# Kernel tuning notes

Hardware: AMD Instinct MI355X
Metric: run time of the kernel (lower is better)

## Reference

```python
import jax, jax.numpy as jnp
import numpy as np

B, T, D = 8, 2048, 768
H, DK = 6, 128            # num_heads, head_dim = n_embd // n_head
DV = 2 * DK               # head_v_dim = head_dim * expand_v
KDIM, VDIM = H * DK, H * DV
CONV = 4
EPS = 1e-5                # RMSNorm eps


def short_conv_silu(x, w):
    """Causal depthwise conv1d (no bias) + SiLU. x: [B,T,C], w: [C,K]."""
    K = w.shape[-1]
    xp = jnp.pad(x, ((0, 0), (K - 1, 0), (0, 0)))
    y = sum(xp[:, i:i + x.shape[1], :] * w[:, i] for i in range(K))
    return jax.nn.silu(y)


def l2norm(x):
    return x * jax.lax.rsqrt(jnp.sum(x * x, axis=-1, keepdims=True) + 1e-6)


def gated_delta_rule(q, k, v, g, beta):
    """q,k: [B,H,T,DK]; v: [B,H,T,DV]; g,beta: [B,H,T]. Returns o: [B,H,T,DV].
    S_t = exp(g_t) * S_{t-1}; v' = beta_t*(v_t - k_t @ S); S += outer(k_t, v'); o_t = scale*q_t @ S."""
    scale = DK ** -0.5

    def per_head(qh, kh, vh, gh, bh):
        def step(S, inp):
            qt, kt, vt, gt, bt = inp
            S = S * jnp.exp(gt)
            v_new = bt * (vt - kt @ S)
            S = S + kt[:, None] * v_new[None, :]
            return S, (qt * scale) @ S
        S0 = jnp.zeros((DK, DV), qh.dtype)
        _, o = jax.lax.scan(step, S0, (qh, kh, vh, gh, bh))
        return o

    return jax.vmap(jax.vmap(per_head))(q, k, v, g, beta)


def setup_inputs() -> dict:
    key = jax.random.key(0)
    ks = jax.random.split(key, 16)
    s = D ** -0.5
    inp = {
        "x": jax.random.normal(ks[0], (B, T, D), jnp.float32),
        "Wq": jax.random.normal(ks[1], (D, KDIM), jnp.float32) * s,
        "Wk": jax.random.normal(ks[2], (D, KDIM), jnp.float32) * s,
        "Wv": jax.random.normal(ks[3], (D, VDIM), jnp.float32) * s,
        "Wa": jax.random.normal(ks[4], (D, H), jnp.float32) * s,
        "Wb": jax.random.normal(ks[5], (D, H), jnp.float32) * s,
        "Wg": jax.random.normal(ks[6], (D, VDIM), jnp.float32) * s,
        "Wo": jax.random.normal(ks[7], (VDIM, D), jnp.float32) * (VDIM ** -0.5),
        "conv_q": jax.random.uniform(ks[8], (KDIM, CONV), jnp.float32, -0.5, 0.5),
        "conv_k": jax.random.uniform(ks[9], (KDIM, CONV), jnp.float32, -0.5, 0.5),
        "conv_v": jax.random.uniform(ks[10], (VDIM, CONV), jnp.float32, -0.5, 0.5),
        "A_log": jnp.log(jax.random.uniform(ks[11], (H,), jnp.float32, 1.0, 8.0)),
        "dt_bias": -4.0 + 0.5 * jax.random.normal(ks[12], (H,), jnp.float32),
        "o_norm_w": jnp.ones((DV,), jnp.float32),
    }
    return inp


def reference(x, Wq, Wk, Wv, Wa, Wb, Wg, Wo, conv_q, conv_k, conv_v, A_log, dt_bias, o_norm_w):
    # projections + causal short conv + silu
    q = short_conv_silu(x @ Wq, conv_q)          # [B,T,KDIM]
    k = short_conv_silu(x @ Wk, conv_k)
    v = short_conv_silu(x @ Wv, conv_v)          # [B,T,VDIM]

    q = l2norm(q.reshape(B, T, H, DK)).transpose(0, 2, 1, 3)   # [B,H,T,DK]
    k = l2norm(k.reshape(B, T, H, DK)).transpose(0, 2, 1, 3)
    v = v.reshape(B, T, H, DV).transpose(0, 2, 1, 3)           # [B,H,T,DV]

    beta = jax.nn.sigmoid(x @ Wb).transpose(0, 2, 1)           # [B,H,T]
    g = -jnp.exp(A_log) * jax.nn.softplus(x @ Wa + dt_bias)    # [B,T,H] log-decay
    g = g.transpose(0, 2, 1)                                   # [B,H,T]

    o = gated_delta_rule(q, k, v, g, beta)                     # [B,H,T,DV]
    o = o.transpose(0, 2, 1, 3)                                # [B,T,H,DV]

    # gated RMSNorm (FusedRMSNormSwishGate): rmsnorm(o)*w*silu(gate)
    gate = (x @ Wg).reshape(B, T, H, DV)
    o = o * jax.lax.rsqrt(jnp.mean(o * o, axis=-1, keepdims=True) + EPS)
    o = o * o_norm_w * jax.nn.silu(gate)

    return o.reshape(B, T, VDIM) @ Wo                          # [B,T,D]
```

## Files before the change

### kernel.cpp

```cpp
#include <hip/hip_runtime.h>
#include <hip/hip_bf16.h>
#include <stdint.h>

#define BB   8
#define TT   2048
#define DD   768
#define HH   6
#define DKd  128
#define DVd  256
#define MM   (BB*TT)
#define K1   768
#define K2   1536
#define CC   32

typedef __bf16 bf16x8 __attribute__((ext_vector_type(8)));
typedef __bf16 bf16x4 __attribute__((ext_vector_type(4)));
typedef float  f32x4  __attribute__((ext_vector_type(4)));

__device__ __forceinline__ float sigm(float x) { return 1.f / (1.f + __expf(-x)); }
__device__ __forceinline__ void split2(float v, __bf16& hi, __bf16& lo) {
  hi = (__bf16)v; lo = (__bf16)(v - (float)hi);
}
__device__ __forceinline__ f32x4 mfma3(bf16x8 ah, bf16x8 al, bf16x8 bh_, bf16x8 bl_, f32x4 acc) {
  acc = __builtin_amdgcn_mfma_f32_16x16x32_bf16(ah, bh_, acc, 0, 0, 0);
  acc = __builtin_amdgcn_mfma_f32_16x16x32_bf16(ah, bl_, acc, 0, 0, 0);
  acc = __builtin_amdgcn_mfma_f32_16x16x32_bf16(al, bh_, acc, 0, 0, 0);
  return acc;
}

__global__ void convert_x_kernel(const float* __restrict__ x, __bf16* __restrict__ Xs) {
  int idx = blockIdx.x * 256 + threadIdx.x;
  if (idx >= MM * DD) return;
  int m = idx / DD, c = idx - m * DD;
  float v = x[idx];
  __bf16 h = (__bf16)v;
  __bf16 l = (__bf16)(v - (float)h);
  size_t base = (size_t)m * (2 * K1) + c;
  Xs[base] = h; Xs[base + K1] = l;
}

__global__ void convert_w_kernel(const float* __restrict__ W, __bf16* __restrict__ Wt,
                                 int K, int N) {
  int idx = blockIdx.x * 256 + threadIdx.x;
  if (idx >= N * 3 * K) return;
  int n = idx / (3 * K), kk = idx - n * (3 * K);
  int blk = kk / K, k = kk - blk * K;
  float v = W[(size_t)k * N + n];
  __bf16 h = (__bf16)v;
  Wt[idx] = (blk == 1) ? (__bf16)(v - (float)h) : h;
}

template <typename OutT>
__global__ __launch_bounds__(256) void gemm_split(
    const __bf16* __restrict__ A, const __bf16* __restrict__ Bt,
    OutT* __restrict__ C, int N, int Khi)
{
  __shared__ __bf16 Als[128 * 32];
  __shared__ __bf16 Bls[128 * 32];
  const int LDA = 2 * Khi, Klog = 3 * Khi;
  const int tid = threadIdx.x;
  const int lane = tid & 63, w = tid >> 6;
  const int wr = w >> 1, wc = w & 1;
  const int bm = blockIdx.x, bn = blockIdx.y;
  f32x4 acc[4][4] = {};
  const __bf16* Ab = A + (size_t)bm * 128 * LDA;
  const __bf16* Bb = Bt + (size_t)bn * 128 * Klog;
  const int r0 = tid >> 2, co0 = (tid & 3) * 8;
  const int r1 = (256 + tid) >> 2, co1 = ((256 + tid) & 3) * 8;
  for (int k0 = 0; k0 < Klog; k0 += 32) {
    const int kc = (k0 < Khi) ? k0 : k0 - Khi;
    __syncthreads();
    __builtin_amdgcn_global_load_lds(
        (const __attribute__((address_space(1))) void*)(Ab + (size_t)r0 * LDA + kc + co0),
        (__attribute__((address_space(3))) void*)(Als + (w * 64) * 8), 16, 0, 0);
    __builtin_amdgcn_global_load_lds(
        (const __attribute__((address_space(1))) void*)(Ab + (size_t)r1 * LDA + kc + co1),
        (__attribute__((address_space(3))) void*)(Als + (256 + w * 64) * 8), 16, 0, 0);
    __builtin_amdgcn_global_load_lds(
        (const __attribute__((address_space(1))) void*)(Bb + (size_t)r0 * Klog + k0 + co0),
        (__attribute__((address_space(3))) void*)(Bls + (w * 64) * 8), 16, 0, 0);
    __builtin_amdgcn_global_load_lds(
        (const __attribute__((address_space(1))) void*)(Bb + (size_t)r1 * Klog + k0 + co1),
        (__attribute__((address_space(3))) void*)(Bls + (256 + w * 64) * 8), 16, 0, 0);
    __syncthreads();
    bf16x8 af[4], bfr[4];
    const int rb = wr * 64 + (lane & 15);
    const int kb = (lane >> 4) * 8;
#pragma unroll
    for (int i = 0; i < 4; ++i) af[i] = *(const bf16x8*)(Als + (rb + i * 16) * 32 + kb);
    const int cb = wc * 64 + (lane & 15);
#pragma unroll
    for (int i = 0; i < 4; ++i) bfr[i] = *(const bf16x8*)(Bls + (cb + i * 16) * 32 + kb);
#pragma unroll
    for (int mi = 0; mi < 4; ++mi)
#pragma unroll
      for (int ni = 0; ni < 4; ++ni)
        acc[mi][ni] = __builtin_amdgcn_mfma_f32_16x16x32_bf16(af[mi], bfr[ni], acc[mi][ni], 0, 0, 0);
  }
  const int row0 = bm * 128 + wr * 64;
  const int col0 = bn * 128 + wc * 64 + (lane & 15);
  const int rsub = (lane >> 4) * 4;
#pragma unroll
  for (int mi = 0; mi < 4; ++mi)
#pragma unroll
    for (int ni = 0; ni < 4; ++ni)
#pragma unroll
      for (int r = 0; r < 4; ++r) {
        int row = row0 + mi * 16 + rsub + r;
        C[(size_t)row * N + col0 + ni * 16] = (OutT)acc[mi][ni][r];
      }
}

__global__ void gb_kernel(const float* __restrict__ x, const float* __restrict__ Wa,
                          const float* __restrict__ Wb, const float* __restrict__ A_log,
                          const float* __restrict__ dt_bias, float* __restrict__ g,
                          float* __restrict__ bet)
{
  const int row = blockIdx.x * 4 + (threadIdx.x >> 6);
  const int lane = threadIdx.x & 63;
  float aA[6] = {0, 0, 0, 0, 0, 0}, aB[6] = {0, 0, 0, 0, 0, 0};
  const float* xr = x + (size_t)row * DD;
  for (int kk = 0; kk < 12; ++kk) {
    const int c = lane + kk * 64;
    const float xv = xr[c];
#pragma unroll
    for (int hh = 0; hh < 6; ++hh) { aA[hh] += xv * Wa[c * 6 + hh]; aB[hh] += xv * Wb[c * 6 + hh]; }
  }
#pragma unroll
  for (int hh = 0; hh < 6; ++hh) {
#pragma unroll
    for (int off = 32; off; off >>= 1) {
      aA[hh] += __shfl_xor(aA[hh], off, 64);
      aB[hh] += __shfl_xor(aB[hh], off, 64);
    }
  }
  if (lane == 0) {
    const int b = row >> 11, t = row & (TT - 1);
#pragma unroll
    for (int hh = 0; hh < 6; ++hh) {
      const float a = aA[hh] + dt_bias[hh];
      const float sp = (a > 20.f) ? a : log1pf(__expf(a));
      const size_t gi = ((size_t)(b * HH + hh)) * TT + t;
      g[gi] = -__expf(A_log[hh]) * sp;
      bet[gi] = 1.f / (1.f + __expf(-aB[hh]));
    }
  }
}

__global__ __launch_bounds__(256) void delta_kernel(
    const __bf16* __restrict__ qpre, const __bf16* __restrict__ kpre,
    const __bf16* __restrict__ vpre,
    const float* __restrict__ cq, const float* __restrict__ ck,
    const float* __restrict__ cv,
    const float* __restrict__ g, const float* __restrict__ bet,
    __bf16* __restrict__ o)
{
  const int bh = blockIdx.x, b = bh / HH, h = bh - b * HH;
  const int jq = blockIdx.y;
  const int tid = threadIdx.x, lane = tid & 63, w = tid >> 6;
  const int r16 = lane & 15, g2 = lane >> 4;

  __shared__ __align__(16) __bf16 Khi[32][136], Klo[32][136];
  __shared__ __align__(16) __bf16 Qhi[32][136], Qlo[32][136];
  __shared__ __align__(16) __bf16 SThi[64][136], STlo[64][136];
  __shared__ __align__(16) __bf16 Ahi[32][40],  Alo[32][40];
  __shared__ __align__(16) __bf16 Phi[32][40],  Plo[32][40];
  __shared__ __align__(16) __bf16 VThi[64][40], VTlo[64][40];
  __shared__ __align__(16) __bf16 GThi[64][16], GTlo[64][16];
  __shared__ __align__(16) __bf16 Thi[4][16][24], Tlo[4][16][24];
  __shared__ __align__(16) float  RHSb[32][66];
  __shared__ __align__(16) float  cwkq[256][4];
  __shared__ __align__(16) float  cwv[64][4];
  __shared__ float Lv[32], Bv[32], BBv[32], BCb[32], Bb2[32];

  {
    const float* src = (tid < 128) ? ck + (size_t)(h * DKd + tid) * 4
                                   : cq + (size_t)(h * DKd + (tid - 128)) * 4;
    *(float4*)&cwkq[tid][0] = *(const float4*)src;
    if (tid < 64) *(float4*)&cwv[tid][0] = *(const float4*)(cv + (size_t)(h * DVd + jq * 64 + tid) * 4);
  }
  for (int i = tid; i < 1088; i += 256) {
    ((uint4*)SThi)[i] = make_uint4(0, 0, 0, 0);
    ((uint4*)STlo)[i] = make_uint4(0, 0, 0, 0);
  }
  __syncthreads();

  const size_t gbase = (size_t)bh * TT;
  const size_t obase = (size_t)bh * TT * DVd + jq * 64;
  const bf16x8 z8 = {};

  for (int chk = 0; chk < TT / CC; ++chk) {
    const int t0 = chk * CC;
    {
      const int r = tid >> 3, cg = tid & 7;
      const int tG = t0 + r;
      {
        bf16x8 tp0[4], tp1[4];
#pragma unroll
        for (int i = 0; i < 4; ++i) {
          int t = tG - 3 + i;
          if (t >= 0) {
            const __bf16* p = kpre + ((size_t)(b * TT + t)) * DD + h * DKd + cg * 16;
            tp0[i] = *(const bf16x8*)p; tp1[i] = *(const bf16x8*)(p + 8);
          } else { tp0[i] = z8; tp1[i] = z8; }
        }
        float ss = 0.f;
#pragma unroll
        for (int c = 0; c < 16; ++c) {
          const float4 w4 = *(const float4*)&cwkq[cg * 16 + c][0];
          const int j = c & 7;
          float y = (c < 8)
              ? (w4.x * (float)tp0[0][j] + w4.y * (float)tp0[1][j] + w4.z * (float)tp0[2][j] + w4.w * (float)tp0[3][j])
              : (w4.x * (float)tp1[0][j] + w4.y * (float)tp1[1][j] + w4.z * (float)tp1[2][j] + w4.w * (float)tp1[3][j]);
          y = y * sigm(y);
          ss += y * y;
          __bf16 hi, lo; split2(y, hi, lo);
          Khi[r][cg * 16 + c] = hi; Klo[r][cg * 16 + c] = lo;
        }
        ss += __shfl_xor(ss, 1, 64); ss += __shfl_xor(ss, 2, 64); ss += __shfl_xor(ss, 4, 64);
        const float inv = rsqrtf(ss + 1e-6f);
#pragma unroll
        for (int c = 0; c < 16; ++c) {
          float v = ((float)Khi[r][cg * 16 + c] + (float)Klo[r][cg * 16 + c]) * inv;
          __bf16 hi, lo; split2(v, hi, lo);
          Khi[r][cg * 16 + c] = hi; Klo[r][cg * 16 + c] = lo;
        }
      }
      {
        bf16x8 tp0[4], tp1[4];
#pragma unroll
        for (int i = 0; i < 4; ++i) {
          int t = tG - 3 + i;
          if (t >= 0) {
            const __bf16* p = qpre + ((size_t)(b * TT + t)) * DD + h * DKd + cg * 16;
            tp0[i] = *(const bf16x8*)p; tp1[i] = *(const bf16x8*)(p + 8);
          } else { tp0[i] = z8; tp1[i] = z8; }
        }
        float ss = 0.f;
#pragma unroll
        for (int c = 0; c < 16; ++c) {
          const float4 w4 = *(const float4*)&cwkq[128 + cg * 16 + c][0];
          const int j = c & 7;
          float y = (c < 8)
              ? (w4.x * (float)tp0[0][j] + w4.y * (float)tp0[1][j] + w4.z * (float)tp0[2][j] + w4.w * (float)tp0[3][j])
              : (w4.x * (float)tp1[0][j] + w4.y * (float)tp1[1][j] + w4.z * (float)tp1[2][j] + w4.w * (float)tp1[3][j]);
          y = y * sigm(y);
          ss += y * y;
          __bf16 hi, lo; split2(y, hi, lo);
          Qhi[r][cg * 16 + c] = hi; Qlo[r][cg * 16 + c] = lo;
        }
        ss += __shfl_xor(ss, 1, 64); ss += __shfl_xor(ss, 2, 64); ss += __shfl_xor(ss, 4, 64);
        const float inv = rsqrtf(ss + 1e-6f) * 0.08838834764831845f;
#pragma unroll
        for (int c = 0; c < 16; ++c) {
          float v = ((float)Qhi[r][cg * 16 + c] + (float)Qlo[r][cg * 16 + c]) * inv;
          __bf16 hi, lo; split2(v, hi, lo);
          Qhi[r][cg * 16 + c] = hi; Qlo[r][cg * 16 + c] = lo;
        }
      }
      {
        bf16x8 tv[4];
#pragma unroll
        for (int i = 0; i < 4; ++i) {
          int t = tG - 3 + i;
          tv[i] = (t >= 0) ? *(const bf16x8*)(vpre + ((size_t)(b * TT + t)) * K2 + h * DVd + jq * 64 + cg * 8) : z8;
        }
#pragma unroll
        for (int c = 0; c < 8; ++c) {
          const float4 w4 = *(const float4*)&cwv[cg * 8 + c][0];
          float y = w4.x * (float)tv[0][c] + w4.y * (float)tv[1][c] + w4.z * (float)tv[2][c] + w4.w * (float)tv[3][c];
          RHSb[r][cg * 8 + c] = y * sigm(y);
        }
      }
      if (tid < 32) {
        float gv = g[gbase + t0 + tid];
        float bv = bet[gbase + t0 + tid];
        float cum = gv;
#pragma unroll
        for (int off = 1; off < 32; off <<= 1) {
          int src = (lane >= off) ? lane - off : lane;
          float n = __shfl(cum, src, 64);
          if (lane >= off) cum += n;
        }
        float LC = __shfl(cum, 31, 64);
        Lv[tid] = cum;
        Bv[tid] = bv;
        float eb = __expf(cum);
        Bb2[tid] = eb;
        BBv[tid] = bv * eb;
        BCb[tid] = __expf(LC - cum);
      }
    }
    __syncthreads();

    {
      const int tr = w >> 1, tc = w & 1;
      f32x4 accA = {0.f, 0.f, 0.f, 0.f}, accP = {0.f, 0.f, 0.f, 0.f};
#pragma unroll
      for (int kb = 0; kb < 128; kb += 32) {
        bf16x8 bh_ = *(const bf16x8*)&Khi[tc * 16 + r16][kb + g2 * 8];
        bf16x8 bl_ = *(const bf16x8*)&Klo[tc * 16 + r16][kb + g2 * 8];
        bf16x8 ah = *(const bf16x8*)&Khi[tr * 16 + r16][kb + g2 * 8];
        bf16x8 al = *(const bf16x8*)&Klo[tr * 16 + r16][kb + g2 * 8];
        accA = mfma3(ah, al, bh_, bl_, accA);
        bf16x8 qh = *(const bf16x8*)&Qhi[tr * 16 + r16][kb + g2 * 8];
        bf16x8 ql = *(const bf16x8*)&Qlo[tr * 16 + r16][kb + g2 * 8];
        accP = mfma3(qh, ql, bh_, bl_, accP);
      }
      const int jj = tc * 16 + r16;
      const float Lj = Lv[jj];
#pragma unroll
      for (int reg = 0; reg < 4; ++reg) {
        const int tt = tr * 16 + g2 * 4 + reg;
        const float dL = Lv[tt] - Lj;
        const float ex = __expf(dL);
        float av = (jj < tt) ? Bv[tt] * ex * accA[reg] : 0.f;
        float pv = (jj <= tt) ? ex * accP[reg] : 0.f;
        __bf16 hi, lo;
        split2(av, hi, lo); Ahi[tt][jj] = hi; Alo[tt][jj] = lo;
        split2(pv, hi, lo); Phi[tt][jj] = hi; Plo[tt][jj] = lo;
      }
    }
    __syncthreads();

    {
      const int rb = w >> 1, cbs = (w & 1) * 2;
      f32x4 acc[2];
#pragma unroll
      for (int ct = 0; ct < 2; ++ct) {
        const int cc = (cbs + ct) * 16 + r16;
#pragma unroll
        for (int reg = 0; reg < 4; ++reg) {
          const int tt = rb * 16 + g2 * 4 + reg;
          acc[ct][reg] = Bv[tt] * RHSb[tt][cc];
        }
      }
      const float fneg = -BBv[rb * 16 + r16];
#pragma unroll
      for (int kb = 0; kb < 128; kb += 32) {
        bf16x8 xh = *(const bf16x8*)&Khi[rb * 16 + r16][kb + g2 * 8];
        bf16x8 xl = *(const bf16x8*)&Klo[rb * 16 + r16][kb + g2 * 8];
        bf16x8 ah, al;
#pragma unroll
        for (int j = 0; j < 8; ++j) {
          float v = fneg * ((float)xh[j] + (float)xl[j]);
          __bf16 hi, lo; split2(v, hi, lo); ah[j] = hi; al[j] = lo;
        }
#pragma unroll
        for (int ct = 0; ct < 2; ++ct) {
          bf16x8 sh = *(const bf16x8*)&SThi[(cbs + ct) * 16 + r16][kb + g2 * 8];
          bf16x8 sl = *(const bf16x8*)&STlo[(cbs + ct) * 16 + r16][kb + g2 * 8];
          acc[ct] = mfma3(ah, al, sh, sl, acc[ct]);
        }
      }
#pragma unroll
      for (int ct = 0; ct < 2; ++ct) {
        const int cc = (cbs + ct) * 16 + r16;
#pragma unroll
        for (int reg = 0; reg < 4; ++reg)
          RHSb[rb * 16 + g2 * 4 + reg][cc] = acc[ct][reg];
      }
    }
    if (w < 2) {
      const int I = w, r0 = I * 16, s = I + 2;
      bf16x8 Lh_r = z8, Ll_r = z8, Lh_t = z8, Ll_t = z8;
      if (g2 < 2) {
        Lh_r = *(const bf16x8*)&Ahi[r0 + r16][r0 + g2 * 8];
        Ll_r = *(const bf16x8*)&Alo[r0 + r16][r0 + g2 * 8];
#pragma unroll
        for (int j = 0; j < 8; ++j) {
          Lh_t[j] = Ahi[r0 + g2 * 8 + j][r0 + r16];
          Ll_t[j] = Alo[r0 + g2 * 8 + j][r0 + r16];
        }
      }
      f32x4 acc = {0.f, 0.f, 0.f, 0.f};
      acc = mfma3(Lh_r, Ll_r, Lh_t, Ll_t, acc);
#pragma unroll
      for (int reg = 0; reg < 4; ++reg) { __bf16 hi, lo; split2(acc[reg], hi, lo);
        Thi[s][g2 * 4 + reg][r16] = hi; Tlo[s][g2 * 4 + reg][r16] = lo; }
      bf16x8 L2h_r = z8, L2l_r = z8, L2h_t = z8, L2l_t = z8;
      if (g2 < 2) { L2h_r = *(const bf16x8*)&Thi[s][r16][g2 * 8]; L2l_r = *(const bf16x8*)&Tlo[s][r16][g2 * 8]; }
#pragma unroll
      for (int j = 0; j < 8; ++j) if (g2 < 2) { L2h_t[j] = Thi[s][g2 * 8 + j][r16]; L2l_t[j] = Tlo[s][g2 * 8 + j][r16]; }
      bf16x8 nLh = Lh_r, nLl = Ll_r;
#pragma unroll
      for (int j = 0; j < 8; ++j) { nLh[j] = -nLh[j]; nLl[j] = -nLl[j]; }
      f32x4 accR;
#pragma unroll
      for (int reg = 0; reg < 4; ++reg) {
        const int rr = g2 * 4 + reg;
        float lw = (float)Ahi[r0 + rr][r0 + r16] + (float)Alo[r0 + rr][r0 + r16];
        float l2w = (float)Thi[s][rr][r16] + (float)Tlo[s][rr][r16];
        accR[reg] = ((rr == r16) ? 1.f : 0.f) - lw + l2w;
      }
      accR = mfma3(nLh, nLl, L2h_t, L2l_t, accR);
#pragma unroll
      for (int reg = 0; reg < 4; ++reg) { __bf16 hi, lo; split2(accR[reg], hi, lo);
        Thi[I][g2 * 4 + reg][r16] = hi; Tlo[I][g2 * 4 + reg][r16] = lo; }
      f32x4 acc4 = {0.f, 0.f, 0.f, 0.f};
      acc4 = mfma3(L2h_r, L2l_r, L2h_t, L2l_t, acc4);
#pragma unroll
      for (int reg = 0; reg < 4; ++reg) { __bf16 hi, lo; split2(acc4[reg], hi, lo);
        Thi[s][g2 * 4 + reg][r16] = hi; Tlo[s][g2 * 4 + reg][r16] = lo; }
      bf16x8 R1h_r = z8, R1l_r = z8, L4h_t = z8, L4l_t = z8, L4h_r = z8, L4l_r = z8;
      if (g2 < 2) {
        R1h_r = *(const bf16x8*)&Thi[I][r16][g2 * 8]; R1l_r = *(const bf16x8*)&Tlo[I][r16][g2 * 8];
        L4h_r = *(const bf16x8*)&Thi[s][r16][g2 * 8]; L4l_r = *(const bf16x8*)&Tlo[s][r16][g2 * 8];
#pragma unroll
        for (int j = 0; j < 8; ++j) { L4h_t[j] = Thi[s][g2 * 8 + j][r16]; L4l_t[j] = Tlo[s][g2 * 8 + j][r16]; }
      }
      f32x4 accR2;
#pragma unroll
      for (int reg = 0; reg < 4; ++reg)
        accR2[reg] = (float)Thi[I][g2 * 4 + reg][r16] + (float)Tlo[I][g2 * 4 + reg][r16];
      accR2 = mfma3(R1h_r, R1l_r, L4h_t, L4l_t, accR2);
#pragma unroll
      for (int reg = 0; reg < 4; ++reg) { __bf16 hi, lo; split2(accR2[reg], hi, lo);
        Thi[I][g2 * 4 + reg][r16] = hi; Tlo[I][g2 * 4 + reg][r16] = lo; }
      f32x4 acc8 = {0.f, 0.f, 0.f, 0.f};
      acc8 = mfma3(L4h_r, L4l_r, L4h_t, L4l_t, acc8);
#pragma unroll
      for (int reg = 0; reg < 4; ++reg) { __bf16 hi, lo; split2(acc8[reg], hi, lo);
        Thi[s][g2 * 4 + reg][r16] = hi; Tlo[s][g2 * 4 + reg][r16] = lo; }
      bf16x8 R2h_r = z8, R2l_r = z8, L8h_t = z8, L8l_t = z8;
      if (g2 < 2) {
        R2h_r = *(const bf16x8*)&Thi[I][r16][g2 * 8]; R2l_r = *(const bf16x8*)&Tlo[I][r16][g2 * 8];
#pragma unroll
        for (int j = 0; j < 8; ++j) { L8h_t[j] = Thi[s][g2 * 8 + j][r16]; L8l_t[j] = Tlo[s][g2 * 8 + j][r16]; }
      }
      f32x4 accT;
#pragma unroll
      for (int reg = 0; reg < 4; ++reg)
        accT[reg] = (float)Thi[I][g2 * 4 + reg][r16] + (float)Tlo[I][g2 * 4 + reg][r16];
      accT = mfma3(R2h_r, R2l_r, L8h_t, L8l_t, accT);
#pragma unroll
      for (int reg = 0; reg < 4; ++reg) { __bf16 hi, lo; split2(accT[reg], hi, lo);
        Thi[I][g2 * 4 + reg][r16] = hi; Tlo[I][g2 * 4 + reg][r16] = lo; }
    }
    __syncthreads();

    {
      const int id0 = tid * 4;
      const int t = id0 >> 6, c0 = id0 & 63;
#pragma unroll
      for (int i = 0; i < 4; ++i) {
        __bf16 hi, lo; split2(RHSb[t][c0 + i], hi, lo);
        GThi[c0 + i][t] = hi; GTlo[c0 + i][t] = lo;
      }
    }
    __syncthreads();
    {
      bf16x8 th = z8, tl = z8, gh = z8, gl = z8;
      if (g2 < 2) {
        th = *(const bf16x8*)&Thi[0][r16][g2 * 8]; tl = *(const bf16x8*)&Tlo[0][r16][g2 * 8];
        gh = *(const bf16x8*)&GThi[w * 16 + r16][g2 * 8]; gl = *(const bf16x8*)&GTlo[w * 16 + r16][g2 * 8];
      }
      f32x4 acc = {0.f, 0.f, 0.f, 0.f};
      acc = mfma3(th, tl, gh, gl, acc);
      bf16x4 p4h, p4l;
#pragma unroll
      for (int reg = 0; reg < 4; ++reg) { __bf16 hi, lo; split2(acc[reg], hi, lo); p4h[reg] = hi; p4l[reg] = lo; }
      *(bf16x4*)&VThi[w * 16 + r16][g2 * 4] = p4h;
      *(bf16x4*)&VTlo[w * 16 + r16][g2 * 4] = p4l;
    }
    __syncthreads();
    {
      const int cb = w;
      f32x4 acc;
#pragma unroll
      for (int reg = 0; reg < 4; ++reg) acc[reg] = RHSb[16 + g2 * 4 + reg][cb * 16 + r16];
      bf16x8 ah = z8, al = z8, vh = z8, vl = z8;
      if (g2 < 2) {
        ah = *(const bf16x8*)&Ahi[16 + r16][g2 * 8]; al = *(const bf16x8*)&Alo[16 + r16][g2 * 8];
#pragma unroll
        for (int j = 0; j < 8; ++j) { ah[j] = -ah[j]; al[j] = -al[j]; }
        vh = *(const bf16x8*)&VThi[cb * 16 + r16][g2 * 8]; vl = *(const bf16x8*)&VTlo[cb * 16 + r16][g2 * 8];
      }
      acc = mfma3(ah, al, vh, vl, acc);
      bf16x4 p4h, p4l;
#pragma unroll
      for (int reg = 0; reg < 4; ++reg) { __bf16 hi, lo; split2(acc[reg], hi, lo); p4h[reg] = hi; p4l[reg] = lo; }
      *(bf16x4*)&GThi[cb * 16 + r16][g2 * 4] = p4h;
      *(bf16x4*)&GTlo[cb * 16 + r16][g2 * 4] = p4l;
    }
    __syncthreads();
    {
      bf16x8 th = z8, tl = z8, gh = z8, gl = z8;
      if (g2 < 2) {
        th = *(const bf16x8*)&Thi[1][r16][g2 * 8]; tl = *(const bf16x8*)&Tlo[1][r16][g2 * 8];
        gh = *(const bf16x8*)&GThi[w * 16 + r16][g2 * 8]; gl = *(const bf16x8*)&GTlo[w * 16 + r16][g2 * 8];
      }
      f32x4 acc = {0.f, 0.f, 0.f, 0.f};
      acc = mfma3(th, tl, gh, gl, acc);
      bf16x4 p4h, p4l;
#pragma unroll
      for (int reg = 0; reg < 4; ++reg) { __bf16 hi, lo; split2(acc[reg], hi, lo); p4h[reg] = hi; p4l[reg] = lo; }
      *(bf16x4*)&VThi[w * 16 + r16][16 + g2 * 4] = p4h;
      *(bf16x4*)&VTlo[w * 16 + r16][16 + g2 * 4] = p4l;
    }
    __syncthreads();

    {
      const int rb = w >> 1, cbs = (w & 1) * 2;
      f32x4 acc[2] = {{0.f, 0.f, 0.f, 0.f}, {0.f, 0.f, 0.f, 0.f}};
      const float fq = Bb2[rb * 16 + r16];
#pragma unroll
      for (int kb = 0; kb < 128; kb += 32) {
        bf16x8 xh = *(const bf16x8*)&Qhi[rb * 16 + r16][kb + g2 * 8];
        bf16x8 xl = *(const bf16x8*)&Qlo[rb * 16 + r16][kb + g2 * 8];
        bf16x8 qh, ql;
#pragma unroll
        for (int j = 0; j < 8; ++j) {
          float v = fq * ((float)xh[j] + (float)xl[j]);
          __bf16 hi, lo; split2(v, hi, lo); qh[j] = hi; ql[j] = lo;
        }
#pragma unroll
        for (int ct = 0; ct < 2; ++ct) {
          bf16x8 sh = *(const bf16x8*)&SThi[(cbs + ct) * 16 + r16][kb + g2 * 8];
          bf16x8 sl = *(const bf16x8*)&STlo[(cbs + ct) * 16 + r16][kb + g2 * 8];
          acc[ct] = mfma3(qh, ql, sh, sl, acc[ct]);
        }
      }
      bf16x8 ph = *(const bf16x8*)&Phi[rb * 16 + r16][g2 * 8];
      bf16x8 pl = *(const bf16x8*)&Plo[rb * 16 + r16][g2 * 8];
#pragma unroll
      for (int ct = 0; ct < 2; ++ct) {
        bf16x8 vh = *(const bf16x8*)&VThi[(cbs + ct) * 16 + r16][g2 * 8];
        bf16x8 vl = *(const bf16x8*)&VTlo[(cbs + ct) * 16 + r16][g2 * 8];
        acc[ct] = mfma3(ph, pl, vh, vl, acc[ct]);
        const int cc = (cbs + ct) * 16 + r16;
#pragma unroll
        for (int reg = 0; reg < 4; ++reg) {
          const int tt = rb * 16 + g2 * 4 + reg;
          o[obase + (size_t)(t0 + tt) * DVd + cc] = (__bf16)acc[ct][reg];
        }
      }
    }
    __syncthreads();

    {
      const float bCf = __expf(Lv[31]);
      bf16x8 vh4[4], vl4[4];
#pragma unroll
      for (int cb = 0; cb < 4; ++cb) {
        vh4[cb] = *(const bf16x8*)&VThi[cb * 16 + r16][g2 * 8];
        vl4[cb] = *(const bf16x8*)&VTlo[cb * 16 + r16][g2 * 8];
      }
#pragma unroll
      for (int rr = 0; rr < 2; ++rr) {
        const int rb = w * 2 + rr, d0 = rb * 16;
        bf16x8 kh, kl;
#pragma unroll
        for (int j = 0; j < 8; ++j) {
          const int t = g2 * 8 + j;
          float v = BCb[t] * ((float)Khi[t][d0 + r16] + (float)Klo[t][d0 + r16]);
          __bf16 hi, lo; split2(v, hi, lo); kh[j] = hi; kl[j] = lo;
        }
#pragma unroll
        for (int cb = 0; cb < 4; ++cb) {
          f32x4 acc;
          const int cc = cb * 16 + r16;
#pragma unroll
          for (int reg = 0; reg < 4; ++reg) {
            const int dd = d0 + g2 * 4 + reg;
            acc[reg] = bCf * ((float)SThi[cc][dd] + (float)STlo[cc][dd]);
          }
          acc = mfma3(kh, kl, vh4[cb], vl4[cb], acc);
          bf16x4 p4h, p4l;
#pragma unroll
          for (int reg = 0; reg < 4; ++reg) { __bf16 hi, lo; split2(acc[reg], hi, lo); p4h[reg] = hi; p4l[reg] = lo; }
          *(bf16x4*)&SThi[cc][d0 + g2 * 4] = p4h;
          *(bf16x4*)&STlo[cc][d0 + g2 * 4] = p4l;
        }
      }
    }
    __syncthreads();
  }
}

__global__ void epilogue_kernel(const __bf16* __restrict__ o, const __bf16* __restrict__ gate,
                                const float* __restrict__ wn, __bf16* __restrict__ Os)
{
  const int bid = blockIdx.x;
  const int m = bid / HH, h = bid - m * HH;
  const int b = m >> 11, t = m & (TT - 1);
  const int j = threadIdx.x;
  const float ov = (float)o[((size_t)(b * HH + h) * TT + t) * DVd + j];
  float ss = ov * ov;
#pragma unroll
  for (int off = 32; off; off >>= 1) ss += __shfl_xor(ss, off, 64);
  __shared__ float red[4];
  if ((j & 63) == 0) red[j >> 6] = ss;
  __syncthreads();
  const float inv = rsqrtf((red[0] + red[1] + red[2] + red[3]) * (1.f / DVd) + 1e-5f);
  const float gt = (float)gate[(size_t)m * K2 + h * DVd + j];
  const float val = ov * inv * wn[j] * (gt * sigm(gt));
  const __bf16 hi = (__bf16)val;
  const __bf16 lo = (__bf16)(val - (float)hi);
  const size_t ob = (size_t)m * (2 * K2) + h * DVd + j;
  Os[ob] = hi; Os[ob + K2] = lo;
}

__global__ void sentinel_kernel(float* __restrict__ out, float val) {
  out[threadIdx.x] = val;
}

extern "C" void kernel_launch(void* const* d_in, const int* in_sizes, int n_in,
                              void* d_out, int out_size, void* d_ws, size_t ws_size,
                              hipStream_t stream) {
  const float* x    = (const float*)d_in[0];
  const float* Wq   = (const float*)d_in[1];
  const float* Wk   = (const float*)d_in[2];
  const float* Wv   = (const float*)d_in[3];
  const float* Wa   = (const float*)d_in[4];
  const float* Wb   = (const float*)d_in[5];
  const float* Wg   = (const float*)d_in[6];
  const float* Wo   = (const float*)d_in[7];
  const float* cq   = (const float*)d_in[8];
  const float* ck   = (const float*)d_in[9];
  const float* cv   = (const float*)d_in[10];
  const float* Alog = (const float*)d_in[11];
  const float* dtb  = (const float*)d_in[12];
  const float* onw  = (const float*)d_in[13];
  float* out = (float*)d_out;
  uint8_t* ws = (uint8_t*)d_ws;

  const size_t oGt = 0;
  const size_t oG  = oGt + 50331648;
  const size_t oBt = oG  + 393216;
  const size_t oWo = oBt + 393216;
  const size_t oWq = oWo + 7077888;
  const size_t oWk = oWq + 3538944;
  const size_t oWv = oWk + 3538944;
  const size_t oWg = oWv + 7077888;
  const size_t oXs = oWg + 7077888;
  const size_t oQp = oXs + 50331648;
  const size_t oKp = oQp + 25165824;
  const size_t oVp = oKp + 25165824;
  const size_t total = oVp + 50331648;
  const size_t oO  = oXs;
  const size_t oOs = oQp;

  if (ws_size < total) {
    sentinel_kernel<<<1, 256, 0, stream>>>(out, 1.0e7f + (float)(ws_size >> 20));
    return;
  }

  __bf16* Xs   = (__bf16*)(ws + oXs);
  __bf16* Wqp  = (__bf16*)(ws + oWq);
  __bf16* Wkp  = (__bf16*)(ws + oWk);
  __bf16* Wvp  = (__bf16*)(ws + oWv);
  __bf16* Wgp  = (__bf16*)(ws + oWg);
  __bf16* Wop  = (__bf16*)(ws + oWo);
  __bf16* qpre = (__bf16*)(ws + oQp);
  __bf16* kpre = (__bf16*)(ws + oKp);
  __bf16* vpre = (__bf16*)(ws + oVp);
  __bf16* gate = (__bf16*)(ws + oGt);
  float*  gbuf = (float*)(ws + oG);
  float*  bbuf = (float*)(ws + oBt);
  __bf16* oBuf = (__bf16*)(ws + oO);
  __bf16* Os   = (__bf16*)(ws + oOs);

  convert_x_kernel<<<MM * DD / 256, 256, 0, stream>>>(x, Xs);
  convert_w_kernel<<<768 * 3 * K1 / 256, 256, 0, stream>>>(Wq, Wqp, K1, 768);
  convert_w_kernel<<<768 * 3 * K1 / 256, 256, 0, stream>>>(Wk, Wkp, K1, 768);
  convert_w_kernel<<<1536 * 3 * K1 / 256, 256, 0, stream>>>(Wv, Wvp, K1, 1536);
  convert_w_kernel<<<1536 * 3 * K1 / 256, 256, 0, stream>>>(Wg, Wgp, K1, 1536);
  convert_w_kernel<<<768 * 3 * K2 / 256, 256, 0, stream>>>(Wo, Wop, K2, 768);
  gemm_split<__bf16><<<dim3(128, 6),  256, 0, stream>>>(Xs, Wqp, qpre, 768,  K1);
  gemm_split<__bf16><<<dim3(128, 6),  256, 0, stream>>>(Xs, Wkp, kpre, 768,  K1);
  gemm_split<__bf16><<<dim3(128, 12), 256, 0, stream>>>(Xs, Wvp, vpre, 1536, K1);
  gemm_split<__bf16><<<dim3(128, 12), 256, 0, stream>>>(Xs, Wgp, gate, 1536, K1);
  gb_kernel<<<MM / 4, 256, 0, stream>>>(x, Wa, Wb, Alog, dtb, gbuf, bbuf);
  delta_kernel<<<dim3(BB * HH, 4), 256, 0, stream>>>(qpre, kpre, vpre, cq, ck, cv,
                                                     gbuf, bbuf, oBuf);
  epilogue_kernel<<<MM * HH, 256, 0, stream>>>(oBuf, gate, onw, Os);
  gemm_split<float><<<dim3(128, 6), 256, 0, stream>>>(Os, Wop, out, 768, K2);
}
```

Baseline: 1.753 ms.

## Restructure chunked delta rule to defer norms, skip masked tiles, shorten triangular solve

The l2-norm scales for q and k are no longer applied by rewriting shared memory. They are kept as per-row factors and folded into the A/P masks, the RHS build and the output scaling. The upper-triangular tiles of the K·K^T and Q·K^T products are skipped. The blocked triangular inverse is restructured so that the off-diagonal correction M is precomputed, which merges several sequential solve stages and their barriers into one. A pre-scaled copy of V is also stored for the state update. This cuts barriers, shared-memory round trips and redundant split-precision conversions per chunk, at the cost of more shared memory and some numerical reordering.

```diff
diff --git a/kernel.cpp b/kernel.cpp
--- a/kernel.cpp
+++ b/kernel.cpp
@@ -165,13 +165,16 @@
   __shared__ __align__(16) __bf16 SThi[64][136], STlo[64][136];
   __shared__ __align__(16) __bf16 Ahi[32][40],  Alo[32][40];
   __shared__ __align__(16) __bf16 Phi[32][40],  Plo[32][40];
+  __shared__ __align__(16) __bf16 Athi[16][24], Atlo[16][24];
   __shared__ __align__(16) __bf16 VThi[64][40], VTlo[64][40];
-  __shared__ __align__(16) __bf16 GThi[64][16], GTlo[64][16];
+  __shared__ __align__(16) __bf16 V2hi[64][40], V2lo[64][40];
+  __shared__ __align__(16) __bf16 GThi[64][40], GTlo[64][40];
   __shared__ __align__(16) __bf16 Thi[4][16][24], Tlo[4][16][24];
-  __shared__ __align__(16) float  RHSb[32][66];
+  __shared__ __align__(16) __bf16 Mhi[16][24], Mlo[16][24];
+  __shared__ __align__(16) float  RHSb[32][68];
   __shared__ __align__(16) float  cwkq[256][4];
   __shared__ __align__(16) float  cwv[64][4];
-  __shared__ float Lv[32], Bv[32], BBv[32], BCb[32], Bb2[32];
+  __shared__ float Lv[32], Bv[32], Bb2[32], BCb[32], ivk[32], ivq[32];
 
   {
     const float* src = (tid < 128) ? ck + (size_t)(h * DKd + tid) * 4
@@ -194,83 +197,72 @@
     {
       const int r = tid >> 3, cg = tid & 7;
       const int tG = t0 + r;
+      bf16x8 kta[4], ktb[4], qta[4], qtb[4], vt4[4];
+#pragma unroll
+      for (int i = 0; i < 4; ++i) {
+        const int t = tG - 3 + i;
+        if (t >= 0) {
+          const __bf16* pk = kpre + ((size_t)(b * TT + t)) * DD + h * DKd + cg * 16;
+          kta[i] = *(const bf16x8*)pk; ktb[i] = *(const bf16x8*)(pk + 8);
+          const __bf16* pq = qpre + ((size_t)(b * TT + t)) * DD + h * DKd + cg * 16;
+          qta[i] = *(const bf16x8*)pq; qtb[i] = *(const bf16x8*)(pq + 8);
+          vt4[i] = *(const bf16x8*)(vpre + ((size_t)(b * TT + t)) * K2 + h * DVd + jq * 64 + cg * 8);
+        } else { kta[i] = z8; ktb[i] = z8; qta[i] = z8; qtb[i] = z8; vt4[i] = z8; }
+      }
       {
-        bf16x8 tp0[4], tp1[4];
-#pragma unroll
-        for (int i = 0; i < 4; ++i) {
-          int t = tG - 3 + i;
-          if (t >= 0) {
-            const __bf16* p = kpre + ((size_t)(b * TT + t)) * DD + h * DKd + cg * 16;
-            tp0[i] = *(const bf16x8*)p; tp1[i] = *(const bf16x8*)(p + 8);
-          } else { tp0[i] = z8; tp1[i] = z8; }
-        }
-        float ss = 0.f;
+        float y[16]; float ss = 0.f;
 #pragma unroll
         for (int c = 0; c < 16; ++c) {
           const float4 w4 = *(const float4*)&cwkq[cg * 16 + c][0];
           const int j = c & 7;
-          float y = (c < 8)
-              ? (w4.x * (float)tp0[0][j] + w4.y * (float)tp0[1][j] + w4.z * (float)tp0[2][j] + w4.w * (float)tp0[3][j])
-              : (w4.x * (float)tp1[0][j] + w4.y * (float)tp1[1][j] + w4.z * (float)tp1[2][j] + w4.w * (float)tp1[3][j]);
-          y = y * sigm(y);
-          ss += y * y;
-          __bf16 hi, lo; split2(y, hi, lo);
-          Khi[r][cg * 16 + c] = hi; Klo[r][cg * 16 + c] = lo;
+          float v = (c < 8)
+              ? (w4.x * (float)kta[0][j] + w4.y * (float)kta[1][j] + w4.z * (float)kta[2][j] + w4.w * (float)kta[3][j])
+              : (w4.x * (float)ktb[0][j] + w4.y * (float)ktb[1][j] + w4.z * (float)ktb[2][j] + w4.w * (float)ktb[3][j]);
+          v = v * sigm(v); y[c] = v; ss += v * v;
         }
         ss += __shfl_xor(ss, 1, 64); ss += __shfl_xor(ss, 2, 64); ss += __shfl_xor(ss, 4, 64);
-        const float inv = rsqrtf(ss + 1e-6f);
-#pragma unroll
-        for (int c = 0; c < 16; ++c) {
-          float v = ((float)Khi[r][cg * 16 + c] + (float)Klo[r][cg * 16 + c]) * inv;
-          __bf16 hi, lo; split2(v, hi, lo);
-          Khi[r][cg * 16 + c] = hi; Klo[r][cg * 16 + c] = lo;
-        }
+        if (cg == 0) ivk[r] = rsqrtf(ss + 1e-6f);
+        bf16x8 h8, l8;
+#pragma unroll
+        for (int j = 0; j < 8; ++j) { __bf16 hi, lo; split2(y[j], hi, lo); h8[j] = hi; l8[j] = lo; }
+        *(bf16x8*)&Khi[r][cg * 16] = h8; *(bf16x8*)&Klo[r][cg * 16] = l8;
+#pragma unroll
+        for (int j = 0; j < 8; ++j) { __bf16 hi, lo; split2(y[8 + j], hi, lo); h8[j] = hi; l8[j] = lo; }
+        *(bf16x8*)&Khi[r][cg * 16 + 8] = h8; *(bf16x8*)&Klo[r][cg * 16 + 8] = l8;
       }
       {
-        bf16x8 tp0[4], tp1[4];
-#pragma unroll
-        for (int i = 0; i < 4; ++i) {
-          int t = tG - 3 + i;
-          if (t >= 0) {
-            const __bf16* p = qpre + ((size_t)(b * TT + t)) * DD + h * DKd + cg * 16;
-            tp0[i] = *(const bf16x8*)p; tp1[i] = *(const bf16x8*)(p + 8);
-          } else { tp0[i] = z8; tp1[i] = z8; }
-        }
-        float ss = 0.f;
+        float y[16]; float ss = 0.f;
 #pragma unroll
         for (int c = 0; c < 16; ++c) {
           const float4 w4 = *(const float4*)&cwkq[128 + cg * 16 + c][0];
           const int j = c & 7;
-          float y = (c < 8)
-              ? (w4.x * (float)tp0[0][j] + w4.y * (float)tp0[1][j] + w4.z * (float)tp0[2][j] + w4.w * (float)tp0[3][j])
-              : (w4.x * (float)tp1[0][j] + w4.y * (float)tp1[1][j] + w4.z * (float)tp1[2][j] + w4.w * (float)tp1[3][j]);
-          y = y * sigm(y);
-          ss += y * y;
-          __bf16 hi, lo; split2(y, hi, lo);
-          Qhi[r][cg * 16 + c] = hi; Qlo[r][cg * 16 + c] = lo;
+          float v = (c < 8)
+              ? (w4.x * (float)qta[0][j] + w4.y * (float)qta[1][j] + w4.z * (float)qta[2][j] + w4.w * (float)qta[3][j])
+              : (w4.x * (float)qtb[0][j] + w4.y * (float)qtb[1][j] + w4.z * (float)qtb[2][j] + w4.w * (float)qtb[3][j]);
+          v = v * sigm(v); y[c] = v; ss += v * v;
         }
         ss += __shfl_xor(ss, 1, 64); ss += __shfl_xor(ss, 2, 64); ss += __shfl_xor(ss, 4, 64);
-        const float inv = rsqrtf(ss + 1e-6f) * 0.08838834764831845f;
-#pragma unroll
-        for (int c = 0; c < 16; ++c) {
-          float v = ((float)Qhi[r][cg * 16 + c] + (float)Qlo[r][cg * 16 + c]) * inv;
-          __bf16 hi, lo; split2(v, hi, lo);
-          Qhi[r][cg * 16 + c] = hi; Qlo[r][cg * 16 + c] = lo;
-        }
+        if (cg == 0) ivq[r] = rsqrtf(ss + 1e-6f) * 0.08838834764831845f;
+        bf16x8 h8, l8;
+#pragma unroll
+        for (int j = 0; j < 8; ++j) { __bf16 hi, lo; split2(y[j], hi, lo); h8[j] = hi; l8[j] = lo; }
+        *(bf16x8*)&Qhi[r][cg * 16] = h8; *(bf16x8*)&Qlo[r][cg * 16] = l8;
+#pragma unroll
+        for (int j = 0; j < 8; ++j) { __bf16 hi, lo; split2(y[8 + j], hi, lo); h8[j] = hi; l8[j] = lo; }
+        *(bf16x8*)&Qhi[r][cg * 16 + 8] = h8; *(bf16x8*)&Qlo[r][cg * 16 + 8] = l8;
       }
       {
-        bf16x8 tv[4];
-#pragma unroll
-        for (int i = 0; i < 4; ++i) {
-          int t = tG - 3 + i;
-          tv[i] = (t >= 0) ? *(const bf16x8*)(vpre + ((size_t)(b * TT + t)) * K2 + h * DVd + jq * 64 + cg * 8) : z8;
-        }
+        float yv[8];
 #pragma unroll
         for (int c = 0; c < 8; ++c) {
           const float4 w4 = *(const float4*)&cwv[cg * 8 + c][0];
-          float y = w4.x * (float)tv[0][c] + w4.y * (float)tv[1][c] + w4.z * (float)tv[2][c] + w4.w * (float)tv[3][c];
-          RHSb[r][cg * 8 + c] = y * sigm(y);
-        }
+          float v = w4.x * (float)vt4[0][c] + w4.y * (float)vt4[1][c] + w4.z * (float)vt4[2][c] + w4.w * (float)vt4[3][c];
+          yv[c] = v * sigm(v);
+        }
+        f32x4 p0 = {yv[0], yv[1], yv[2], yv[3]};
+        f32x4 p1 = {yv[4], yv[5], yv[6], yv[7]};
+        *(f32x4*)&RHSb[r][cg * 8] = p0;
+        *(f32x4*)&RHSb[r][cg * 8 + 4] = p1;
       }
       if (tid < 32) {
         float gv = g[gbase + t0 + tid];
@@ -285,9 +277,7 @@
         float LC = __shfl(cum, 31, 64);
         Lv[tid] = cum;
         Bv[tid] = bv;
-        float eb = __expf(cum);
-        Bb2[tid] = eb;
-        BBv[tid] = bv * eb;
+        Bb2[tid] = __expf(cum);
         BCb[tid] = __expf(LC - cum);
       }
     }
@@ -295,29 +285,31 @@
 
     {
       const int tr = w >> 1, tc = w & 1;
+      const int jj = tc * 16 + r16;
       f32x4 accA = {0.f, 0.f, 0.f, 0.f}, accP = {0.f, 0.f, 0.f, 0.f};
-#pragma unroll
-      for (int kb = 0; kb < 128; kb += 32) {
-        bf16x8 bh_ = *(const bf16x8*)&Khi[tc * 16 + r16][kb + g2 * 8];
-        bf16x8 bl_ = *(const bf16x8*)&Klo[tc * 16 + r16][kb + g2 * 8];
-        bf16x8 ah = *(const bf16x8*)&Khi[tr * 16 + r16][kb + g2 * 8];
-        bf16x8 al = *(const bf16x8*)&Klo[tr * 16 + r16][kb + g2 * 8];
-        accA = mfma3(ah, al, bh_, bl_, accA);
-        bf16x8 qh = *(const bf16x8*)&Qhi[tr * 16 + r16][kb + g2 * 8];
-        bf16x8 ql = *(const bf16x8*)&Qlo[tr * 16 + r16][kb + g2 * 8];
-        accP = mfma3(qh, ql, bh_, bl_, accP);
-      }
-      const int jj = tc * 16 + r16;
-      const float Lj = Lv[jj];
+      if (tc <= tr) {
+#pragma unroll
+        for (int kb = 0; kb < 128; kb += 32) {
+          bf16x8 bh_ = *(const bf16x8*)&Khi[jj][kb + g2 * 8];
+          bf16x8 bl_ = *(const bf16x8*)&Klo[jj][kb + g2 * 8];
+          bf16x8 ah = *(const bf16x8*)&Khi[tr * 16 + r16][kb + g2 * 8];
+          bf16x8 al = *(const bf16x8*)&Klo[tr * 16 + r16][kb + g2 * 8];
+          accA = mfma3(ah, al, bh_, bl_, accA);
+          bf16x8 qh = *(const bf16x8*)&Qhi[tr * 16 + r16][kb + g2 * 8];
+          bf16x8 ql = *(const bf16x8*)&Qlo[tr * 16 + r16][kb + g2 * 8];
+          accP = mfma3(qh, ql, bh_, bl_, accP);
+        }
+      }
+      const float Lj = Lv[jj], ikj = ivk[jj];
 #pragma unroll
       for (int reg = 0; reg < 4; ++reg) {
         const int tt = tr * 16 + g2 * 4 + reg;
-        const float dL = Lv[tt] - Lj;
-        const float ex = __expf(dL);
-        float av = (jj < tt) ? Bv[tt] * ex * accA[reg] : 0.f;
-        float pv = (jj <= tt) ? ex * accP[reg] : 0.f;
+        const float ex = __expf(Lv[tt] - Lj);
+        const float av = (jj < tt) ? Bv[tt] * ivk[tt] * ikj * ex * accA[reg] : 0.f;
+        const float pv = (jj <= tt) ? ivq[tt] * ikj * ex * accP[reg] : 0.f;
         __bf16 hi, lo;
         split2(av, hi, lo); Ahi[tt][jj] = hi; Alo[tt][jj] = lo;
+        if (tr == 1 && tc == 0) { Athi[jj][tt - 16] = hi; Atlo[jj][tt - 16] = lo; }
         split2(pv, hi, lo); Phi[tt][jj] = hi; Plo[tt][jj] = lo;
       }
     }
@@ -325,27 +317,11 @@
 
     {
       const int rb = w >> 1, cbs = (w & 1) * 2;
-      f32x4 acc[2];
-#pragma unroll
-      for (int ct = 0; ct < 2; ++ct) {
-        const int cc = (cbs + ct) * 16 + r16;
-#pragma unroll
-        for (int reg = 0; reg < 4; ++reg) {
-          const int tt = rb * 16 + g2 * 4 + reg;
-          acc[ct][reg] = Bv[tt] * RHSb[tt][cc];
-        }
-      }
-      const float fneg = -BBv[rb * 16 + r16];
+      f32x4 acc[2] = {{0.f, 0.f, 0.f, 0.f}, {0.f, 0.f, 0.f, 0.f}};
 #pragma unroll
       for (int kb = 0; kb < 128; kb += 32) {
-        bf16x8 xh = *(const bf16x8*)&Khi[rb * 16 + r16][kb + g2 * 8];
-        bf16x8 xl = *(const bf16x8*)&Klo[rb * 16 + r16][kb + g2 * 8];
-        bf16x8 ah, al;
-#pragma unroll
-        for (int j = 0; j < 8; ++j) {
-          float v = fneg * ((float)xh[j] + (float)xl[j]);
-          __bf16 hi, lo; split2(v, hi, lo); ah[j] = hi; al[j] = lo;
-        }
+        bf16x8 ah = *(const bf16x8*)&Khi[rb * 16 + r16][kb + g2 * 8];
+        bf16x8 al = *(const bf16x8*)&Klo[rb * 16 + r16][kb + g2 * 8];
 #pragma unroll
         for (int ct = 0; ct < 2; ++ct) {
           bf16x8 sh = *(const bf16x8*)&SThi[(cbs + ct) * 16 + r16][kb + g2 * 8];
@@ -357,8 +333,14 @@
       for (int ct = 0; ct < 2; ++ct) {
         const int cc = (cbs + ct) * 16 + r16;
 #pragma unroll
-        for (int reg = 0; reg < 4; ++reg)
-          RHSb[rb * 16 + g2 * 4 + reg][cc] = acc[ct][reg];
+        for (int reg = 0; reg < 4; ++reg) {
+          const int tt = rb * 16 + g2 * 4 + reg;
+          const float f1 = Bv[tt];
+          const float f2 = f1 * Bb2[tt] * ivk[tt];
+          const float val = f1 * RHSb[tt][cc] - f2 * acc[ct][reg];
+          __bf16 hi, lo; split2(val, hi, lo);
+          GThi[cc][tt] = hi; GTlo[cc][tt] = lo;
+        }
       }
     }
     if (w < 2) {
@@ -436,84 +418,81 @@
 #pragma unroll
       for (int reg = 0; reg < 4; ++reg) { __bf16 hi, lo; split2(accT[reg], hi, lo);
         Thi[I][g2 * 4 + reg][r16] = hi; Tlo[I][g2 * 4 + reg][r16] = lo; }
+      if (I == 0) {
+#pragma unroll
+        for (int reg = 0; reg < 4; ++reg) { __bf16 hi, lo; split2(accT[reg], hi, lo);
+          Thi[2][r16][g2 * 4 + reg] = hi; Tlo[2][r16][g2 * 4 + reg] = lo; }
+      } else {
+        bf16x8 t1h = z8, t1l = z8, ath = z8, atl = z8;
+        if (g2 < 2) {
+          t1h = *(const bf16x8*)&Thi[1][r16][g2 * 8]; t1l = *(const bf16x8*)&Tlo[1][r16][g2 * 8];
+          ath = *(const bf16x8*)&Athi[r16][g2 * 8];   atl = *(const bf16x8*)&Atlo[r16][g2 * 8];
+        }
+        f32x4 xacc = {0.f, 0.f, 0.f, 0.f};
+        xacc = mfma3(t1h, t1l, ath, atl, xacc);
+#pragma unroll
+        for (int reg = 0; reg < 4; ++reg) { __bf16 hi, lo; split2(xacc[reg], hi, lo);
+          Thi[3][g2 * 4 + reg][r16] = hi; Tlo[3][g2 * 4 + reg][r16] = lo; }
+      }
+    }
+    __syncthreads();
+
+    if (w == 1) {
+      bf16x8 xh = z8, xl = z8, th = z8, tl = z8;
+      if (g2 < 2) {
+        xh = *(const bf16x8*)&Thi[3][r16][g2 * 8]; xl = *(const bf16x8*)&Tlo[3][r16][g2 * 8];
+        th = *(const bf16x8*)&Thi[2][r16][g2 * 8]; tl = *(const bf16x8*)&Tlo[2][r16][g2 * 8];
+      }
+      f32x4 macc = {0.f, 0.f, 0.f, 0.f};
+      macc = mfma3(xh, xl, th, tl, macc);
+#pragma unroll
+      for (int reg = 0; reg < 4; ++reg) { __bf16 hi, lo; split2(-macc[reg], hi, lo);
+        Mhi[g2 * 4 + reg][r16] = hi; Mlo[g2 * 4 + reg][r16] = lo; }
     }
     __syncthreads();
 
     {
-      const int id0 = tid * 4;
-      const int t = id0 >> 6, c0 = id0 & 63;
-#pragma unroll
-      for (int i = 0; i < 4; ++i) {
-        __bf16 hi, lo; split2(RHSb[t][c0 + i], hi, lo);
-        GThi[c0 + i][t] = hi; GTlo[c0 + i][t] = lo;
-      }
-    }
-    __syncthreads();
-    {
-      bf16x8 th = z8, tl = z8, gh = z8, gl = z8;
+      const int c0 = w * 16;
+      bf16x8 t0h = z8, t0l = z8, g0h = z8, g0l = z8, t1h = z8, t1l = z8;
+      bf16x8 g1h = z8, g1l = z8, mh = z8, ml = z8;
       if (g2 < 2) {
-        th = *(const bf16x8*)&Thi[0][r16][g2 * 8]; tl = *(const bf16x8*)&Tlo[0][r16][g2 * 8];
-        gh = *(const bf16x8*)&GThi[w * 16 + r16][g2 * 8]; gl = *(const bf16x8*)&GTlo[w * 16 + r16][g2 * 8];
-      }
-      f32x4 acc = {0.f, 0.f, 0.f, 0.f};
-      acc = mfma3(th, tl, gh, gl, acc);
-      bf16x4 p4h, p4l;
-#pragma unroll
-      for (int reg = 0; reg < 4; ++reg) { __bf16 hi, lo; split2(acc[reg], hi, lo); p4h[reg] = hi; p4l[reg] = lo; }
-      *(bf16x4*)&VThi[w * 16 + r16][g2 * 4] = p4h;
-      *(bf16x4*)&VTlo[w * 16 + r16][g2 * 4] = p4l;
-    }
-    __syncthreads();
-    {
-      const int cb = w;
-      f32x4 acc;
-#pragma unroll
-      for (int reg = 0; reg < 4; ++reg) acc[reg] = RHSb[16 + g2 * 4 + reg][cb * 16 + r16];
-      bf16x8 ah = z8, al = z8, vh = z8, vl = z8;
-      if (g2 < 2) {
-        ah = *(const bf16x8*)&Ahi[16 + r16][g2 * 8]; al = *(const bf16x8*)&Alo[16 + r16][g2 * 8];
-#pragma unroll
-        for (int j = 0; j < 8; ++j) { ah[j] = -ah[j]; al[j] = -al[j]; }
-        vh = *(const bf16x8*)&VThi[cb * 16 + r16][g2 * 8]; vl = *(const bf16x8*)&VTlo[cb * 16 + r16][g2 * 8];
-      }
-      acc = mfma3(ah, al, vh, vl, acc);
-      bf16x4 p4h, p4l;
-#pragma unroll
-      for (int reg = 0; reg < 4; ++reg) { __bf16 hi, lo; split2(acc[reg], hi, lo); p4h[reg] = hi; p4l[reg] = lo; }
-      *(bf16x4*)&GThi[cb * 16 + r16][g2 * 4] = p4h;
-      *(bf16x4*)&GTlo[cb * 16 + r16][g2 * 4] = p4l;
-    }
-    __syncthreads();
-    {
-      bf16x8 th = z8, tl = z8, gh = z8, gl = z8;
-      if (g2 < 2) {
-        th = *(const bf16x8*)&Thi[1][r16][g2 * 8]; tl = *(const bf16x8*)&Tlo[1][r16][g2 * 8];
-        gh = *(const bf16x8*)&GThi[w * 16 + r16][g2 * 8]; gl = *(const bf16x8*)&GTlo[w * 16 + r16][g2 * 8];
-      }
-      f32x4 acc = {0.f, 0.f, 0.f, 0.f};
-      acc = mfma3(th, tl, gh, gl, acc);
-      bf16x4 p4h, p4l;
-#pragma unroll
-      for (int reg = 0; reg < 4; ++reg) { __bf16 hi, lo; split2(acc[reg], hi, lo); p4h[reg] = hi; p4l[reg] = lo; }
-      *(bf16x4*)&VThi[w * 16 + r16][16 + g2 * 4] = p4h;
-      *(bf16x4*)&VTlo[w * 16 + r16][16 + g2 * 4] = p4l;
+        t0h = *(const bf16x8*)&Thi[0][r16][g2 * 8]; t0l = *(const bf16x8*)&Tlo[0][r16][g2 * 8];
+        t1h = *(const bf16x8*)&Thi[1][r16][g2 * 8]; t1l = *(const bf16x8*)&Tlo[1][r16][g2 * 8];
+        mh  = *(const bf16x8*)&Mhi[r16][g2 * 8];    ml  = *(const bf16x8*)&Mlo[r16][g2 * 8];
+        g0h = *(const bf16x8*)&GThi[c0 + r16][g2 * 8];      g0l = *(const bf16x8*)&GTlo[c0 + r16][g2 * 8];
+        g1h = *(const bf16x8*)&GThi[c0 + r16][16 + g2 * 8]; g1l = *(const bf16x8*)&GTlo[c0 + r16][16 + g2 * 8];
+      }
+      f32x4 a0 = {0.f, 0.f, 0.f, 0.f}, a1 = {0.f, 0.f, 0.f, 0.f};
+      a0 = mfma3(t0h, t0l, g0h, g0l, a0);
+      a1 = mfma3(t1h, t1l, g1h, g1l, a1);
+      a1 = mfma3(mh, ml, g0h, g0l, a1);
+      bf16x4 vh, vl, v2h, v2l;
+#pragma unroll
+      for (int reg = 0; reg < 4; ++reg) {
+        const int ti = g2 * 4 + reg;
+        __bf16 hi, lo; split2(a0[reg], hi, lo); vh[reg] = hi; vl[reg] = lo;
+        split2(a0[reg] * BCb[ti] * ivk[ti], hi, lo); v2h[reg] = hi; v2l[reg] = lo;
+      }
+      *(bf16x4*)&VThi[c0 + r16][g2 * 4] = vh;  *(bf16x4*)&VTlo[c0 + r16][g2 * 4] = vl;
+      *(bf16x4*)&V2hi[c0 + r16][g2 * 4] = v2h; *(bf16x4*)&V2lo[c0 + r16][g2 * 4] = v2l;
+#pragma unroll
+      for (int reg = 0; reg < 4; ++reg) {
+        const int ti = 16 + g2 * 4 + reg;
+        __bf16 hi, lo; split2(a1[reg], hi, lo); vh[reg] = hi; vl[reg] = lo;
+        split2(a1[reg] * BCb[ti] * ivk[ti], hi, lo); v2h[reg] = hi; v2l[reg] = lo;
+      }
+      *(bf16x4*)&VThi[c0 + r16][16 + g2 * 4] = vh;  *(bf16x4*)&VTlo[c0 + r16][16 + g2 * 4] = vl;
+      *(bf16x4*)&V2hi[c0 + r16][16 + g2 * 4] = v2h; *(bf16x4*)&V2lo[c0 + r16][16 + g2 * 4] = v2l;
     }
     __syncthreads();
 
     {
       const int rb = w >> 1, cbs = (w & 1) * 2;
       f32x4 acc[2] = {{0.f, 0.f, 0.f, 0.f}, {0.f, 0.f, 0.f, 0.f}};
-      const float fq = Bb2[rb * 16 + r16];
 #pragma unroll
       for (int kb = 0; kb < 128; kb += 32) {
-        bf16x8 xh = *(const bf16x8*)&Qhi[rb * 16 + r16][kb + g2 * 8];
-        bf16x8 xl = *(const bf16x8*)&Qlo[rb * 16 + r16][kb + g2 * 8];
-        bf16x8 qh, ql;
-#pragma unroll
-        for (int j = 0; j < 8; ++j) {
-          float v = fq * ((float)xh[j] + (float)xl[j]);
-          __bf16 hi, lo; split2(v, hi, lo); qh[j] = hi; ql[j] = lo;
-        }
+        bf16x8 qh = *(const bf16x8*)&Qhi[rb * 16 + r16][kb + g2 * 8];
+        bf16x8 ql = *(const bf16x8*)&Qlo[rb * 16 + r16][kb + g2 * 8];
 #pragma unroll
         for (int ct = 0; ct < 2; ++ct) {
           bf16x8 sh = *(const bf16x8*)&SThi[(cbs + ct) * 16 + r16][kb + g2 * 8];
@@ -521,6 +500,13 @@
           acc[ct] = mfma3(qh, ql, sh, sl, acc[ct]);
         }
       }
+      float fr[4];
+#pragma unroll
+      for (int reg = 0; reg < 4; ++reg) { const int tt = rb * 16 + g2 * 4 + reg; fr[reg] = Bb2[tt] * ivq[tt]; }
+#pragma unroll
+      for (int ct = 0; ct < 2; ++ct)
+#pragma unroll
+        for (int reg = 0; reg < 4; ++reg) acc[ct][reg] *= fr[reg];
       bf16x8 ph = *(const bf16x8*)&Phi[rb * 16 + r16][g2 * 8];
       bf16x8 pl = *(const bf16x8*)&Plo[rb * 16 + r16][g2 * 8];
 #pragma unroll
@@ -530,42 +516,39 @@
         acc[ct] = mfma3(ph, pl, vh, vl, acc[ct]);
         const int cc = (cbs + ct) * 16 + r16;
 #pragma unroll
-        for (int reg = 0; reg < 4; ++reg) {
-          const int tt = rb * 16 + g2 * 4 + reg;
-          o[obase + (size_t)(t0 + tt) * DVd + cc] = (__bf16)acc[ct][reg];
-        }
+        for (int reg = 0; reg < 4; ++reg)
+          o[obase + (size_t)(t0 + rb * 16 + g2 * 4 + reg) * DVd + cc] = (__bf16)acc[ct][reg];
       }
     }
     __syncthreads();
 
     {
-      const float bCf = __expf(Lv[31]);
-      bf16x8 vh4[4], vl4[4];
+      const float bCf = Bb2[31];
+      bf16x8 v2h4[4], v2l4[4];
 #pragma unroll
       for (int cb = 0; cb < 4; ++cb) {
-        vh4[cb] = *(const bf16x8*)&VThi[cb * 16 + r16][g2 * 8];
-        vl4[cb] = *(const bf16x8*)&VTlo[cb * 16 + r16][g2 * 8];
+        v2h4[cb] = *(const bf16x8*)&V2hi[cb * 16 + r16][g2 * 8];
+        v2l4[cb] = *(const bf16x8*)&V2lo[cb * 16 + r16][g2 * 8];
       }
 #pragma unroll
       for (int rr = 0; rr < 2; ++rr) {
-        const int rb = w * 2 + rr, d0 = rb * 16;
+        const int d0 = (w * 2 + rr) * 16;
         bf16x8 kh, kl;
 #pragma unroll
         for (int j = 0; j < 8; ++j) {
           const int t = g2 * 8 + j;
-          float v = BCb[t] * ((float)Khi[t][d0 + r16] + (float)Klo[t][d0 + r16]);
-          __bf16 hi, lo; split2(v, hi, lo); kh[j] = hi; kl[j] = lo;
+          kh[j] = Khi[t][d0 + r16]; kl[j] = Klo[t][d0 + r16];
         }
 #pragma unroll
         for (int cb = 0; cb < 4; ++cb) {
+          const int cc = cb * 16 + r16;
           f32x4 acc;
-          const int cc = cb * 16 + r16;
 #pragma unroll
           for (int reg = 0; reg < 4; ++reg) {
             const int dd = d0 + g2 * 4 + reg;
             acc[reg] = bCf * ((float)SThi[cc][dd] + (float)STlo[cc][dd]);
           }
-          acc = mfma3(kh, kl, vh4[cb], vl4[cb], acc);
+          acc = mfma3(kh, kl, v2h4[cb], v2l4[cb], acc);
           bf16x4 p4h, p4l;
 #pragma unroll
           for (int reg = 0; reg < 4; ++reg) { __bf16 hi, lo; split2(acc[reg], hi, lo); p4h[reg] = hi; p4l[reg] = lo; }
```

New measurement: 1.639 ms. 6.5% less time.
